# Optimization experiments

Measured on AMD Instinct MI355X. Metric: run time of the kernel, lower is better.

The kernel has to match this reference:

```python
import jax, jax.numpy as jnp
import numpy as np

EMB = 1024
HEADS = 16
HEAD_DIM = EMB // HEADS
EPS = 1e-5


def setup_inputs() -> dict:
    key = jax.random.key(0)
    ks = jax.random.split(key, 10)
    B, T, D = 2, 2048, EMB
    s = 1.0 / np.sqrt(D)
    inp = {
        "x": jax.random.normal(ks[0], (B, T, D), dtype=jnp.float32),
        "wq": jax.random.normal(ks[1], (D, D), dtype=jnp.float32) * s,
        "bq": jnp.zeros((D,), jnp.float32),
        "wk": jax.random.normal(ks[2], (D, D), dtype=jnp.float32) * s,
        "bk": jnp.zeros((D,), jnp.float32),
        "wv": jax.random.normal(ks[3], (D, D), dtype=jnp.float32) * s,
        "bv": jnp.zeros((D,), jnp.float32),
        "wo": jax.random.normal(ks[4], (D, D), dtype=jnp.float32) * s,
        "bo": jnp.zeros((D,), jnp.float32),
        "gamma": jnp.ones((D,), jnp.float32),
        "beta": jnp.zeros((D,), jnp.float32),
    }
    return inp


def _attention(x, wq, bq, wk, bk, wv, bv, wo, bo, gamma, beta):
    B, T, D = x.shape
    H, Hd = HEADS, HEAD_DIM
    q = (x @ wq + bq).reshape(B, T, H, Hd)
    k = (x @ wk + bk).reshape(B, T, H, Hd)
    v = (x @ wv + bv).reshape(B, T, H, Hd)
    # scores: [B, H, T, T]
    scores = jnp.einsum("bthd,bshd->bhts", q, k) / np.sqrt(Hd)
    attn = jax.nn.softmax(scores, axis=-1)  # dropout is identity in eval
    ctx = jnp.einsum("bhts,bshd->bthd", attn, v).reshape(B, T, D)
    out = ctx @ wo + bo
    y = x + out  # residual (dropout identity)
    mu = jnp.mean(y, axis=-1, keepdims=True)
    var = jnp.var(y, axis=-1, keepdims=True)
    return (y - mu) * jax.lax.rsqrt(var + EPS) * gamma + beta


def reference(x, wq, bq, wk, bk, wv, bv, wo, bo, gamma, beta):
    return _attention(x, wq, bq, wk, bk, wv, bv, wo, bo, gamma, beta)
```

## Files before the change

kernel.cpp:

```cpp
#include <hip/hip_runtime.h>

#define BSZ   2
#define TSEQ  2048
#define DMOD  1024
#define NHEAD 16
#define HDIM  64
#define MROW  (BSZ*TSEQ)
#define LNEPS 1e-5f
#define QSCALE 0.18033688011f

typedef __bf16 bf16x8 __attribute__((ext_vector_type(8)));
typedef float  f32x4  __attribute__((ext_vector_type(4)));
typedef unsigned short us8 __attribute__((ext_vector_type(8)));
typedef unsigned short us4 __attribute__((ext_vector_type(4)));

__device__ __forceinline__ unsigned short f2bf(float f) {
    unsigned u = __float_as_uint(f);
    u += 0x7FFF + ((u >> 16) & 1);
    return (unsigned short)(u >> 16);
}
__device__ __forceinline__ float bf2f(unsigned short u) {
    return __uint_as_float((unsigned)u << 16);
}

__device__ __forceinline__ float fexp2(float x) {
#if __has_builtin(__builtin_amdgcn_exp2f)
    return __builtin_amdgcn_exp2f(x);
#else
    return __expf(x * 0.6931471805599453f);
#endif
}

__device__ __forceinline__ void gld_lds16(const void* g, void* l) {
    __builtin_amdgcn_global_load_lds(
        (const __attribute__((address_space(1))) unsigned int*)g,
        (__attribute__((address_space(3))) unsigned int*)l, 16, 0, 0);
}

__global__ __launch_bounds__(256) void prep_k(
    const float* __restrict__ x,
    const float* __restrict__ wq, const float* __restrict__ wk,
    const float* __restrict__ wv, const float* __restrict__ wo,
    unsigned short* __restrict__ Xb,
    unsigned short* __restrict__ WqkvT, unsigned short* __restrict__ WoT)
{
    const int tid = threadIdx.x;
    if (blockIdx.x < 2048) {
        const size_t i = ((size_t)blockIdx.x * 256 + tid) * 8;
        float4 a = *(const float4*)&x[i];
        float4 b = *(const float4*)&x[i + 4];
        union { unsigned short u[8]; uint4 v; } o;
        o.u[0]=f2bf(a.x); o.u[1]=f2bf(a.y); o.u[2]=f2bf(a.z); o.u[3]=f2bf(a.w);
        o.u[4]=f2bf(b.x); o.u[5]=f2bf(b.y); o.u[6]=f2bf(b.z); o.u[7]=f2bf(b.w);
        *(uint4*)&Xb[i] = o.v;
        return;
    }
    __shared__ float T[64][68];
    const int id = blockIdx.x - 2048;
    const int z  = id >> 8;
    const int bx = id & 15;
    const int by = (id >> 4) & 15;
    const float* W = (z == 0) ? wq : (z == 1) ? wk : (z == 2) ? wv : wo;
    unsigned short* Wt = (z < 3) ? (WqkvT + (size_t)z*1024*1024) : WoT;
    const int lr = tid >> 4, lc = (tid & 15) * 4;
    #pragma unroll
    for (int p = 0; p < 4; ++p) {
        const int kk = p*16 + lr;
        float4 v = *(const float4*)&W[(size_t)(by*64 + kk)*1024 + bx*64 + lc];
        T[lc+0][kk] = v.x; T[lc+1][kk] = v.y; T[lc+2][kk] = v.z; T[lc+3][kk] = v.w;
    }
    __syncthreads();
    #pragma unroll
    for (int p = 0; p < 2; ++p) {
        const int nl = p*32 + (tid >> 3);
        const int kb = (tid & 7) * 8;
        float4 a = *(const float4*)&T[nl][kb];
        float4 b = *(const float4*)&T[nl][kb+4];
        union { unsigned short u[8]; uint4 v; } o;
        o.u[0]=f2bf(a.x); o.u[1]=f2bf(a.y); o.u[2]=f2bf(a.z); o.u[3]=f2bf(a.w);
        o.u[4]=f2bf(b.x); o.u[5]=f2bf(b.y); o.u[6]=f2bf(b.z); o.u[7]=f2bf(b.w);
        *(uint4*)&Wt[(size_t)(bx*64 + nl)*1024 + by*64 + kb] = o.v;
    }
}

struct GemmFrags {
    const unsigned short* Ag[4]; const unsigned short* Bg[4];
    unsigned short *la[4], *lb[4];
    const unsigned short *ap[4][2], *bp[4][2];
};

__device__ __forceinline__ void gemm_setup(
    GemmFrags& F, unsigned short* As, unsigned short* Bs,
    const unsigned short* A, const unsigned short* Bt,
    int bm, int bn, int lda)
{
    const int tid  = threadIdx.x;
    const int wv   = tid >> 6;
    const int lane = tid & 63;
    const int quad = lane >> 4;
    const int l16  = lane & 15;
    const int wm   = wv & 1, wn = wv >> 1;
    const int r_l = lane >> 3;
    const int c_l = lane & 7;
    #pragma unroll
    for (int s = 0; s < 4; ++s) {
        const int i = wv*4 + s;
        const int R = i*8 + r_l;
        const int gc = (c_l ^ (R & 7)) * 8;
        F.Ag[s] = A  + (size_t)(bm + R)*lda + gc;
        F.Bg[s] = Bt + (size_t)(bn + R)*lda + gc;
        F.la[s] = As + i*512;
        F.lb[s] = Bs + i*512;
    }
    #pragma unroll
    for (int t = 0; t < 4; ++t)
        #pragma unroll
        for (int kh = 0; kh < 2; ++kh) {
            const int ra = wm*64 + t*16 + l16;
            const int rb = wn*64 + t*16 + l16;
            F.ap[t][kh] = &As[ra*64 + ((kh*4 + quad) ^ (ra & 7))*8];
            F.bp[t][kh] = &Bs[rb*64 + ((kh*4 + quad) ^ (rb & 7))*8];
        }
}

__device__ __forceinline__ void gemm_kloop(
    GemmFrags& F, f32x4 (&acc)[4][4], int k_begin, int k_end)
{
    for (int k0 = k_begin; k0 < k_end; k0 += 64) {
        __syncthreads();
        #pragma unroll
        for (int s = 0; s < 4; ++s) {
            gld_lds16(F.Ag[s] + k0, F.la[s]);
            gld_lds16(F.Bg[s] + k0, F.lb[s]);
        }
        __syncthreads();
        #pragma unroll
        for (int kh = 0; kh < 2; ++kh) {
            bf16x8 af[4], bfr[4];
            #pragma unroll
            for (int t = 0; t < 4; ++t) {
                af[t]  = *(const bf16x8*)F.ap[t][kh];
                bfr[t] = *(const bf16x8*)F.bp[t][kh];
            }
            #pragma unroll
            for (int i = 0; i < 4; ++i)
                #pragma unroll
                for (int j = 0; j < 4; ++j)
                    acc[i][j] = __builtin_amdgcn_mfma_f32_16x16x32_bf16(af[i], bfr[j], acc[i][j], 0, 0, 0);
        }
    }
}

__global__ __launch_bounds__(256) void gemm_qkv_k(
    const unsigned short* __restrict__ A, const unsigned short* __restrict__ Bt,
    const float* __restrict__ b0, const float* __restrict__ b1,
    const float* __restrict__ b2,
    unsigned short* __restrict__ oQ, unsigned short* __restrict__ oK,
    unsigned short* __restrict__ oV)
{
    __shared__ unsigned short As[128*64];
    __shared__ unsigned short Bs[128*64];
    const int tid  = threadIdx.x;
    const int wv   = tid >> 6;
    const int lane = tid & 63;
    const int quad = lane >> 4;
    const int l16  = lane & 15;
    const int wm   = wv & 1, wn = wv >> 1;
    const int bm = blockIdx.y * 128, bn = blockIdx.x * 128;

    GemmFrags F;
    gemm_setup(F, As, Bs, A, Bt, bm, bn, 1024);

    f32x4 acc[4][4];
    #pragma unroll
    for (int i = 0; i < 4; ++i)
        #pragma unroll
        for (int j = 0; j < 4; ++j) acc[i][j] = (f32x4){0.f,0.f,0.f,0.f};

    gemm_kloop(F, acc, 0, 1024);

    const int seg = bn >> 10;
    const float* bias = (seg == 0) ? b0 : (seg == 1) ? b1 : b2;
    const int cb = bn & 1023;
    if (seg < 2) {
        unsigned short* O = (seg == 0) ? oQ : oK;
        const float sc = (seg == 0) ? QSCALE : 1.0f;
        #pragma unroll
        for (int nt = 0; nt < 4; ++nt) {
            const int col = cb + wn*64 + nt*16 + l16;
            const float bs = bias[col];
            #pragma unroll
            for (int mt = 0; mt < 4; ++mt)
                #pragma unroll
                for (int r = 0; r < 4; ++r) {
                    const int grow = bm + wm*64 + mt*16 + quad*4 + r;
                    O[(size_t)grow*1024 + col] = f2bf((acc[mt][nt][r] + bs) * sc);
                }
        }
    } else {
        #pragma unroll
        for (int nt = 0; nt < 4; ++nt) {
            const int ch = cb + wn*64 + nt*16 + l16;
            const float bs = bias[ch];
            #pragma unroll
            for (int mt = 0; mt < 4; ++mt) {
                const int grow0 = bm + wm*64 + mt*16 + quad*4;
                us4 o;
                #pragma unroll
                for (int r = 0; r < 4; ++r) o[r] = f2bf(acc[mt][nt][r] + bs);
                *(us4*)&oV[(size_t)ch*MROW + grow0] = o;
            }
        }
    }
}

__global__ __launch_bounds__(256) void gemm_proj_k(
    const unsigned short* __restrict__ A, const unsigned short* __restrict__ Bt,
    unsigned short* __restrict__ P)
{
    __shared__ unsigned short As[128*64];
    __shared__ unsigned short Bs[128*64];
    const int tid  = threadIdx.x;
    const int wv   = tid >> 6;
    const int lane = tid & 63;
    const int quad = lane >> 4;
    const int l16  = lane & 15;
    const int wm   = wv & 1, wn = wv >> 1;
    const int bm = blockIdx.y * 128, bn = blockIdx.x * 128;
    const int kz = blockIdx.z;

    GemmFrags F;
    gemm_setup(F, As, Bs, A, Bt, bm, bn, 1024);

    f32x4 acc[4][4];
    #pragma unroll
    for (int i = 0; i < 4; ++i)
        #pragma unroll
        for (int j = 0; j < 4; ++j) acc[i][j] = (f32x4){0.f,0.f,0.f,0.f};

    gemm_kloop(F, acc, kz*512, kz*512 + 512);

    unsigned short* O = P + (size_t)kz*MROW*1024;
    #pragma unroll
    for (int nt = 0; nt < 4; ++nt) {
        const int col = bn + wn*64 + nt*16 + l16;
        #pragma unroll
        for (int mt = 0; mt < 4; ++mt)
            #pragma unroll
            for (int r = 0; r < 4; ++r) {
                const int grow = bm + wm*64 + mt*16 + quad*4 + r;
                O[(size_t)grow*1024 + col] = f2bf(acc[mt][nt][r]);
            }
    }
}

__global__ __launch_bounds__(256, 2) void attn_k(
    const unsigned short* __restrict__ Qg,
    const unsigned short* __restrict__ Kg,
    const unsigned short* __restrict__ Vtg,
    unsigned short* __restrict__ CTX)
{
    __shared__ __align__(16) char lds_raw[51200];
    unsigned short* Qs = (unsigned short*)lds_raw;
    unsigned short* Ks = (unsigned short*)(lds_raw + 18432);
    unsigned short* Vs = (unsigned short*)(lds_raw + 34816);
    float* Od = (float*)lds_raw;
    float* Ld = (float*)(lds_raw + 34816);

    const int tid  = threadIdx.x;
    const int wv   = tid >> 6;
    const int lane = tid & 63;
    const int quad = lane >> 4;
    const int l16  = lane & 15;
    const int wq   = wv & 1;
    const int wk   = wv >> 1;
    const int qb   = blockIdx.x * 128;
    const int h    = blockIdx.y;
    const int b    = blockIdx.z;

    {
        const int row = tid & 127, cb = (tid >> 7) * 32;
        const unsigned short* Qrow = Qg + ((size_t)(b*TSEQ + qb + row))*DMOD + h*HDIM + cb;
        #pragma unroll
        for (int j = 0; j < 4; ++j)
            *(us8*)&Qs[row*72 + cb + j*8] = *(const us8*)&Qrow[j*8];
    }
    __syncthreads();
    bf16x8 qf[4][2];
    #pragma unroll
    for (int nt = 0; nt < 4; ++nt)
        #pragma unroll
        for (int kh = 0; kh < 2; ++kh)
            qf[nt][kh] = *(const bf16x8*)&Qs[(wq*64 + nt*16 + l16)*72 + kh*32 + quad*8];

    const int sr = lane >> 3;
    const int sc = lane & 7;
    const bool isK = (wv < 2);
    const int half = wv & 1;
    const unsigned short* gbase;
    unsigned int goff[8];
    unsigned short* ldst;
    if (isK) {
        gbase = Kg + ((size_t)(b*TSEQ + half*1024))*DMOD + h*HDIM;
        #pragma unroll
        for (int s = 0; s < 8; ++s) {
            const int R = s*8 + sr;
            const int gc = sc ^ ((R ^ (R >> 2)) & 7);
            goff[s] = (unsigned)(R*DMOD + gc*8);
        }
        ldst = Ks + half*4096;
    } else {
        gbase = Vtg + ((size_t)(h*HDIM))*MROW + b*TSEQ + half*1024;
        #pragma unroll
        for (int s = 0; s < 8; ++s) {
            const int D = s*8 + sr;
            const int gc = sc ^ (D & 7);
            goff[s] = (unsigned)(D*MROW + gc*8);
        }
        ldst = Vs + half*4096;
    }
    const size_t gstep = isK ? (size_t)64*DMOD : (size_t)64;

    const int rowA_l = (l16 >> 2)*8 + (l16 & 3);
    const int rowB_l = rowA_l + 4;
    const int swA = (rowA_l ^ (rowA_l >> 2)) & 7;
    const int swB = (rowB_l ^ (rowB_l >> 2)) & 7;
    const unsigned short* KsW = Ks + wk*4096;
    const unsigned short* VsW = Vs + wk*4096;

    bf16x8 onef;
    { union { unsigned short u[8]; bf16x8 v; } o1;
      #pragma unroll
      for (int i = 0; i < 8; ++i) o1.u[i] = 0x3F80;
      onef = o1.v; }

    f32x4 oacc[4][4];
    f32x4 lacc[4];
    #pragma unroll
    for (int dt = 0; dt < 4; ++dt)
        #pragma unroll
        for (int nt = 0; nt < 4; ++nt) oacc[dt][nt] = (f32x4){0.f,0.f,0.f,0.f};
    #pragma unroll
    for (int nt = 0; nt < 4; ++nt) lacc[nt] = (f32x4){0.f,0.f,0.f,0.f};

    for (int it = 0; it < 16; ++it) {
        __syncthreads();
        #pragma unroll
        for (int s = 0; s < 8; ++s)
            gld_lds16(gbase + (size_t)it*gstep + goff[s], ldst + s*512);
        __syncthreads();

        #pragma unroll
        for (int gl = 0; gl < 2; ++gl) {
            const int rA = gl*32 + rowA_l;
            const int rB = gl*32 + rowB_l;
            bf16x8 ka0 = *(const bf16x8*)&KsW[rA*64 + ((quad     ^ swA))*8];
            bf16x8 ka1 = *(const bf16x8*)&KsW[rA*64 + (((4+quad) ^ swA))*8];
            bf16x8 kb0 = *(const bf16x8*)&KsW[rB*64 + ((quad     ^ swB))*8];
            bf16x8 kb1 = *(const bf16x8*)&KsW[rB*64 + (((4+quad) ^ swB))*8];
            bf16x8 vf[4];
            #pragma unroll
            for (int dt = 0; dt < 4; ++dt)
                vf[dt] = *(const bf16x8*)&VsW[(dt*16 + l16)*64 + ((gl*4 + quad) ^ (l16 & 7))*8];

            #pragma unroll
            for (int nt = 0; nt < 4; ++nt) {
                f32x4 z = (f32x4){0.f,0.f,0.f,0.f};
                z = __builtin_amdgcn_mfma_f32_16x16x32_bf16(ka0, qf[nt][0], z, 0, 0, 0);
                f32x4 sA = __builtin_amdgcn_mfma_f32_16x16x32_bf16(ka1, qf[nt][1], z, 0, 0, 0);
                z = (f32x4){0.f,0.f,0.f,0.f};
                z = __builtin_amdgcn_mfma_f32_16x16x32_bf16(kb0, qf[nt][0], z, 0, 0, 0);
                f32x4 sB = __builtin_amdgcn_mfma_f32_16x16x32_bf16(kb1, qf[nt][1], z, 0, 0, 0);

                float eA[4], eB[4];
                #pragma unroll
                for (int r = 0; r < 4; ++r) { eA[r] = fexp2(sA[r]); eB[r] = fexp2(sB[r]); }
                union { unsigned d[4]; bf16x8 v; } up;
                up.d[0] = __builtin_amdgcn_perm(__float_as_uint(eA[1]), __float_as_uint(eA[0]), 0x07060302);
                up.d[1] = __builtin_amdgcn_perm(__float_as_uint(eA[3]), __float_as_uint(eA[2]), 0x07060302);
                up.d[2] = __builtin_amdgcn_perm(__float_as_uint(eB[1]), __float_as_uint(eB[0]), 0x07060302);
                up.d[3] = __builtin_amdgcn_perm(__float_as_uint(eB[3]), __float_as_uint(eB[2]), 0x07060302);
                const bf16x8 pf = up.v;

                lacc[nt] = __builtin_amdgcn_mfma_f32_16x16x32_bf16(onef, pf, lacc[nt], 0, 0, 0);
                #pragma unroll
                for (int dt = 0; dt < 4; ++dt)
                    oacc[dt][nt] = __builtin_amdgcn_mfma_f32_16x16x32_bf16(vf[dt], pf, oacc[dt][nt], 0, 0, 0);
            }
        }
    }

    __syncthreads();
    if (wk == 0) {
        float* od = Od + wq*64*68;
        #pragma unroll
        for (int nt = 0; nt < 4; ++nt) {
            #pragma unroll
            for (int dt = 0; dt < 4; ++dt)
                *(f32x4*)&od[(nt*16 + l16)*68 + dt*16 + quad*4] = oacc[dt][nt];
            if (quad == 0) Ld[wq*64 + nt*16 + l16] = lacc[nt][0];
        }
    }
    __syncthreads();
    if (wk == 1) {
        const float* od = Od + wq*64*68;
        #pragma unroll
        for (int nt = 0; nt < 4; ++nt) {
            const float l = Ld[wq*64 + nt*16 + l16] + lacc[nt][0];
            const float inv = 1.f / l;
            const int q = qb + wq*64 + nt*16 + l16;
            unsigned short* crow = CTX + ((size_t)(b*TSEQ + q))*DMOD + h*HDIM;
            #pragma unroll
            for (int dt = 0; dt < 4; ++dt) {
                f32x4 p = *(const f32x4*)&od[(nt*16 + l16)*68 + dt*16 + quad*4];
                us4 o;
                #pragma unroll
                for (int r = 0; r < 4; ++r) o[r] = f2bf((p[r] + oacc[dt][nt][r]) * inv);
                *(us4*)&crow[dt*16 + quad*4] = o;
            }
        }
    }
}

__global__ __launch_bounds__(256) void red_ln_k(
    const float* __restrict__ x, const unsigned short* __restrict__ P,
    const float* __restrict__ bo,
    const float* __restrict__ gamma, const float* __restrict__ beta,
    float* __restrict__ out)
{
    __shared__ float rs[4], rss[4];
    const int row = blockIdx.x;
    const int tid = threadIdx.x;
    const int c = tid * 4;
    const float4 xv = *(const float4*)&x[(size_t)row*DMOD + c];
    const us4 p0 = *(const us4*)&P[(size_t)row*DMOD + c];
    const us4 p1 = *(const us4*)&P[(size_t)(MROW + row)*DMOD + c];
    const float4 bv4 = *(const float4*)&bo[c];
    const float v0 = xv.x + bf2f(p0[0]) + bf2f(p1[0]) + bv4.x;
    const float v1 = xv.y + bf2f(p0[1]) + bf2f(p1[1]) + bv4.y;
    const float v2 = xv.z + bf2f(p0[2]) + bf2f(p1[2]) + bv4.z;
    const float v3 = xv.w + bf2f(p0[3]) + bf2f(p1[3]) + bv4.w;
    float s  = v0 + v1 + v2 + v3;
    float ss = v0*v0 + v1*v1 + v2*v2 + v3*v3;
    #pragma unroll
    for (int o = 32; o > 0; o >>= 1) {
        s  += __shfl_down(s,  o, 64);
        ss += __shfl_down(ss, o, 64);
    }
    if ((tid & 63) == 0) { rs[tid >> 6] = s; rss[tid >> 6] = ss; }
    __syncthreads();
    s  = rs[0] + rs[1] + rs[2] + rs[3];
    ss = rss[0] + rss[1] + rss[2] + rss[3];
    const float mean = s * (1.f/DMOD);
    const float var  = ss * (1.f/DMOD) - mean*mean;
    const float rstd = rsqrtf(var + LNEPS);
    const float4 gv = *(const float4*)&gamma[c];
    const float4 bv = *(const float4*)&beta[c];
    float4 o;
    o.x = (v0 - mean)*rstd*gv.x + bv.x;
    o.y = (v1 - mean)*rstd*gv.y + bv.y;
    o.z = (v2 - mean)*rstd*gv.z + bv.z;
    o.w = (v3 - mean)*rstd*gv.w + bv.w;
    *(float4*)&out[(size_t)row*DMOD + c] = o;
}

extern "C" void kernel_launch(void* const* d_in, const int* in_sizes, int n_in,
                              void* d_out, int out_size, void* d_ws, size_t ws_size,
                              hipStream_t stream) {
    const float* x     = (const float*)d_in[0];
    const float* wq    = (const float*)d_in[1];
    const float* bq    = (const float*)d_in[2];
    const float* wk    = (const float*)d_in[3];
    const float* bk    = (const float*)d_in[4];
    const float* wvp   = (const float*)d_in[5];
    const float* bvp   = (const float*)d_in[6];
    const float* wo    = (const float*)d_in[7];
    const float* bo    = (const float*)d_in[8];
    const float* gamma = (const float*)d_in[9];
    const float* beta  = (const float*)d_in[10];
    float* out = (float*)d_out;

    unsigned short* Xb    = (unsigned short*)d_ws;
    unsigned short* WqkvT = Xb    + (size_t)MROW*DMOD;
    unsigned short* WoT   = WqkvT + (size_t)3072*1024;
    unsigned short* Qb    = WoT   + (size_t)1024*1024;
    unsigned short* Kb    = Qb    + (size_t)MROW*DMOD;
    unsigned short* VtG   = Kb    + (size_t)MROW*DMOD;
    unsigned short* CTXb  = VtG   + (size_t)DMOD*MROW;
    unsigned short* Pp    = Qb;

    prep_k<<<3072, 256, 0, stream>>>(x, wq, wk, wvp, wo, Xb, WqkvT, WoT);

    gemm_qkv_k<<<dim3(3072/128, MROW/128), 256, 0, stream>>>(
        Xb, WqkvT, bq, bk, bvp, Qb, Kb, VtG);

    attn_k<<<dim3(TSEQ/128, NHEAD, BSZ), 256, 0, stream>>>(Qb, Kb, VtG, CTXb);

    gemm_proj_k<<<dim3(DMOD/128, MROW/128, 2), 256, 0, stream>>>(CTXb, WoT, Pp);

    red_ln_k<<<MROW, 256, 0, stream>>>(x, Pp, bo, gamma, beta, out);
}
```

Before: 196.5 us.

## Rewrite QKV and projection GEMMs as 256x256 double-buffered 8-wave pipelined kernels

Replaces the 128x128 single-buffered GEMM core with a 256x256 tile computed by 512 threads (8 waves). It uses 128 KB of dynamic LDS for double-buffered A/B K-slabs, interleaving async global-to-LDS loads with MFMA phases under barrier scheduling and s_setprio. Block indices are remapped with a grouped swizzle to improve L2 reuse. The intent is to hide global load latency and raise MFMA utilisation. The risks are fewer blocks (192 and 128) on a 256-CU part, lower occupancy from the large LDS footprint, and fragile manual waitcnt accounting.

```diff
diff --git a/kernel.cpp b/kernel.cpp
--- a/kernel.cpp
+++ b/kernel.cpp
@@ -83,173 +83,256 @@
     }
 }
 
-struct GemmFrags {
-    const unsigned short* Ag[4]; const unsigned short* Bg[4];
-    unsigned short *la[4], *lb[4];
-    const unsigned short *ap[4][2], *bp[4][2];
+
+#define PH_SYNC() do { __builtin_amdgcn_s_barrier(); \
+    asm volatile("s_waitcnt lgkmcnt(0)" ::: "memory"); \
+    __builtin_amdgcn_sched_barrier(0); } while (0)
+
+struct Core8 {
+    const unsigned short *sA, *sB;
+    unsigned short *A0w, *A1w, *B0w, *B1w;
+    const unsigned short *fA0, *fA1, *fB0, *fB1;
+    int swz0, swz1;
 };
 
-__device__ __forceinline__ void gemm_setup(
-    GemmFrags& F, unsigned short* As, unsigned short* Bs,
-    const unsigned short* A, const unsigned short* Bt,
-    int bm, int bn, int lda)
-{
-    const int tid  = threadIdx.x;
-    const int wv   = tid >> 6;
-    const int lane = tid & 63;
-    const int quad = lane >> 4;
-    const int l16  = lane & 15;
-    const int wm   = wv & 1, wn = wv >> 1;
-    const int r_l = lane >> 3;
-    const int c_l = lane & 7;
-    #pragma unroll
-    for (int s = 0; s < 4; ++s) {
-        const int i = wv*4 + s;
-        const int R = i*8 + r_l;
-        const int gc = (c_l ^ (R & 7)) * 8;
-        F.Ag[s] = A  + (size_t)(bm + R)*lda + gc;
-        F.Bg[s] = Bt + (size_t)(bn + R)*lda + gc;
-        F.la[s] = As + i*512;
-        F.lb[s] = Bs + i*512;
-    }
-    #pragma unroll
-    for (int t = 0; t < 4; ++t)
-        #pragma unroll
-        for (int kh = 0; kh < 2; ++kh) {
-            const int ra = wm*64 + t*16 + l16;
-            const int rb = wn*64 + t*16 + l16;
-            F.ap[t][kh] = &As[ra*64 + ((kh*4 + quad) ^ (ra & 7))*8];
-            F.bp[t][kh] = &Bs[rb*64 + ((kh*4 + quad) ^ (rb & 7))*8];
-        }
-}
-
-__device__ __forceinline__ void gemm_kloop(
-    GemmFrags& F, f32x4 (&acc)[4][4], int k_begin, int k_end)
-{
-    for (int k0 = k_begin; k0 < k_end; k0 += 64) {
-        __syncthreads();
-        #pragma unroll
-        for (int s = 0; s < 4; ++s) {
-            gld_lds16(F.Ag[s] + k0, F.la[s]);
-            gld_lds16(F.Bg[s] + k0, F.lb[s]);
-        }
-        __syncthreads();
-        #pragma unroll
-        for (int kh = 0; kh < 2; ++kh) {
-            bf16x8 af[4], bfr[4];
-            #pragma unroll
-            for (int t = 0; t < 4; ++t) {
-                af[t]  = *(const bf16x8*)F.ap[t][kh];
-                bfr[t] = *(const bf16x8*)F.bp[t][kh];
-            }
-            #pragma unroll
-            for (int i = 0; i < 4; ++i)
-                #pragma unroll
-                for (int j = 0; j < 4; ++j)
-                    acc[i][j] = __builtin_amdgcn_mfma_f32_16x16x32_bf16(af[i], bfr[j], acc[i][j], 0, 0, 0);
-        }
-    }
-}
-
-__global__ __launch_bounds__(256) void gemm_qkv_k(
+__device__ __forceinline__ void stage2(const unsigned short* s, unsigned short* d) {
+    gld_lds16(s, d);
+    gld_lds16(s + 64*1024, d + 4096);
+}
+
+__device__ __forceinline__ void core_setup(Core8& C, unsigned short* LDS,
+    const unsigned short* A, const unsigned short* Bt, int bm, int bn, int kbase)
+{
+    const int tid = threadIdx.x;
+    const int w = tid >> 6, lane = tid & 63;
+    const int quad = lane >> 4, l16 = lane & 15;
+    const int wm = w >> 2, wn = w & 3;
+    const int r_l = lane >> 3, c_l = lane & 7;
+    C.sA = A  + (size_t)(bm + w*8 + r_l)*1024 + (c_l ^ r_l)*8 + kbase;
+    C.sB = Bt + (size_t)(bn + w*8 + r_l)*1024 + (c_l ^ r_l)*8 + kbase;
+    unsigned short* A0 = LDS;
+    unsigned short* A1 = LDS + 16384;
+    unsigned short* B0 = LDS + 32768;
+    unsigned short* B1 = LDS + 49152;
+    C.A0w = A0 + w*512; C.A1w = A1 + w*512;
+    C.B0w = B0 + w*512; C.B1w = B1 + w*512;
+    C.fA0 = A0 + (wm*128 + l16)*64; C.fA1 = A1 + (wm*128 + l16)*64;
+    C.fB0 = B0 + (wn*64 + l16)*64;  C.fB1 = B1 + (wn*64 + l16)*64;
+    C.swz0 = ( quad      ^ (l16 & 7)) * 8;
+    C.swz1 = ((4 + quad) ^ (l16 & 7)) * 8;
+}
+
+__device__ __forceinline__ void ld_b(const Core8& C, bf16x8 (&bfr)[4][2],
+                                     const unsigned short* fB) {
+    #pragma unroll
+    for (int n = 0; n < 4; ++n) {
+        bfr[n][0] = *(const bf16x8*)(fB + n*1024 + C.swz0);
+        bfr[n][1] = *(const bf16x8*)(fB + n*1024 + C.swz1);
+    }
+}
+
+template<int Q>
+__device__ __forceinline__ void ld_a(const Core8& C, bf16x8 (&af)[2][2],
+                                     const unsigned short* fA) {
+    #pragma unroll
+    for (int dm = 0; dm < 2; ++dm) {
+        af[dm][0] = *(const bf16x8*)(fA + (Q*2+dm)*1024 + C.swz0);
+        af[dm][1] = *(const bf16x8*)(fA + (Q*2+dm)*1024 + C.swz1);
+    }
+}
+
+template<int Q>
+__device__ __forceinline__ void mma_q(f32x4 (&acc)[8][4], bf16x8 (&af)[2][2],
+                                      bf16x8 (&bfr)[4][2]) {
+    __builtin_amdgcn_s_setprio(1);
+    #pragma unroll
+    for (int dm = 0; dm < 2; ++dm)
+        #pragma unroll
+        for (int n = 0; n < 4; ++n) {
+            f32x4 t = acc[Q*2+dm][n];
+            t = __builtin_amdgcn_mfma_f32_16x16x32_bf16(af[dm][0], bfr[n][0], t, 0, 0, 0);
+            t = __builtin_amdgcn_mfma_f32_16x16x32_bf16(af[dm][1], bfr[n][1], t, 0, 0, 0);
+            acc[Q*2+dm][n] = t;
+        }
+    __builtin_amdgcn_s_setprio(0);
+}
+
+template<int NIT>
+__device__ __forceinline__ void core_kloop(const Core8& C, f32x4 (&acc)[8][4])
+{
+    stage2(C.sA,                 C.A0w);
+    stage2(C.sA + 128*1024,      C.A0w + 8192);
+    stage2(C.sB,                 C.B0w);
+    stage2(C.sB + 128*1024,      C.B0w + 8192);
+    stage2(C.sB + 64,            C.B1w);
+    stage2(C.sB + 128*1024 + 64, C.B1w + 8192);
+    asm volatile("s_waitcnt vmcnt(4)" ::: "memory");
+    __builtin_amdgcn_s_barrier();
+
+    bf16x8 bfr[4][2];
+    bf16x8 af[2][2];
+
+    #pragma unroll 1
+    for (int it = 0; it < NIT - 1; ++it) {
+        const int kk = it * 128;
+        ld_b(C, bfr, C.fB0);
+        ld_a<0>(C, af, C.fA0);
+        stage2(C.sA + kk + 64,            C.A1w);
+        stage2(C.sA + 128*1024 + kk + 64, C.A1w + 8192);
+        PH_SYNC();  mma_q<0>(acc, af, bfr);
+        __builtin_amdgcn_s_barrier();
+        ld_a<1>(C, af, C.fA0);
+        stage2(C.sB + kk + 128, C.B0w);
+        PH_SYNC();  mma_q<1>(acc, af, bfr);
+        __builtin_amdgcn_s_barrier();
+        ld_a<2>(C, af, C.fA0);
+        stage2(C.sB + 128*1024 + kk + 128, C.B0w + 8192);
+        PH_SYNC();  mma_q<2>(acc, af, bfr);
+        __builtin_amdgcn_s_barrier();
+        ld_a<3>(C, af, C.fA0);
+        PH_SYNC();  mma_q<3>(acc, af, bfr);
+        asm volatile("s_waitcnt vmcnt(4)" ::: "memory");
+        __builtin_amdgcn_s_barrier();
+        ld_b(C, bfr, C.fB1);
+        ld_a<0>(C, af, C.fA1);
+        stage2(C.sA + kk + 128,            C.A0w);
+        stage2(C.sA + 128*1024 + kk + 128, C.A0w + 8192);
+        PH_SYNC();  mma_q<0>(acc, af, bfr);
+        __builtin_amdgcn_s_barrier();
+        ld_a<1>(C, af, C.fA1);
+        stage2(C.sB + kk + 192, C.B1w);
+        PH_SYNC();  mma_q<1>(acc, af, bfr);
+        __builtin_amdgcn_s_barrier();
+        ld_a<2>(C, af, C.fA1);
+        stage2(C.sB + 128*1024 + kk + 192, C.B1w + 8192);
+        PH_SYNC();  mma_q<2>(acc, af, bfr);
+        __builtin_amdgcn_s_barrier();
+        ld_a<3>(C, af, C.fA1);
+        PH_SYNC();  mma_q<3>(acc, af, bfr);
+        asm volatile("s_waitcnt vmcnt(4)" ::: "memory");
+        __builtin_amdgcn_s_barrier();
+    }
+
+    {
+        const int kk = (NIT - 1) * 128;
+        ld_b(C, bfr, C.fB0);
+        ld_a<0>(C, af, C.fA0);
+        stage2(C.sA + kk + 64,            C.A1w);
+        stage2(C.sA + 128*1024 + kk + 64, C.A1w + 8192);
+        PH_SYNC();  mma_q<0>(acc, af, bfr);
+        __builtin_amdgcn_s_barrier();
+        ld_a<1>(C, af, C.fA0); PH_SYNC(); mma_q<1>(acc, af, bfr); __builtin_amdgcn_s_barrier();
+        ld_a<2>(C, af, C.fA0); PH_SYNC(); mma_q<2>(acc, af, bfr); __builtin_amdgcn_s_barrier();
+        ld_a<3>(C, af, C.fA0); PH_SYNC(); mma_q<3>(acc, af, bfr);
+        asm volatile("s_waitcnt vmcnt(0)" ::: "memory");
+        __builtin_amdgcn_s_barrier();
+        ld_b(C, bfr, C.fB1);
+        ld_a<0>(C, af, C.fA1); PH_SYNC(); mma_q<0>(acc, af, bfr); __builtin_amdgcn_s_barrier();
+        ld_a<1>(C, af, C.fA1); PH_SYNC(); mma_q<1>(acc, af, bfr); __builtin_amdgcn_s_barrier();
+        ld_a<2>(C, af, C.fA1); PH_SYNC(); mma_q<2>(acc, af, bfr); __builtin_amdgcn_s_barrier();
+        ld_a<3>(C, af, C.fA1); PH_SYNC(); mma_q<3>(acc, af, bfr);
+    }
+}
+
+__global__ __launch_bounds__(512, 2) void gemm_qkv_k(
     const unsigned short* __restrict__ A, const unsigned short* __restrict__ Bt,
     const float* __restrict__ b0, const float* __restrict__ b1,
     const float* __restrict__ b2,
     unsigned short* __restrict__ oQ, unsigned short* __restrict__ oK,
     unsigned short* __restrict__ oV)
 {
-    __shared__ unsigned short As[128*64];
-    __shared__ unsigned short Bs[128*64];
-    const int tid  = threadIdx.x;
-    const int wv   = tid >> 6;
-    const int lane = tid & 63;
-    const int quad = lane >> 4;
-    const int l16  = lane & 15;
-    const int wm   = wv & 1, wn = wv >> 1;
-    const int bm = blockIdx.y * 128, bn = blockIdx.x * 128;
-
-    GemmFrags F;
-    gemm_setup(F, As, Bs, A, Bt, bm, bn, 1024);
-
-    f32x4 acc[4][4];
-    #pragma unroll
-    for (int i = 0; i < 4; ++i)
+    extern __shared__ unsigned short LDS[];
+    const int ob = blockIdx.x;
+    const int wg = (ob & 7) * 24 + (ob >> 3);
+    const int by = wg / 12, bx = wg - by*12;
+    const int bm = by * 256, bn = bx * 256;
+
+    Core8 C;
+    core_setup(C, LDS, A, Bt, bm, bn, 0);
+
+    f32x4 acc[8][4];
+    #pragma unroll
+    for (int i = 0; i < 8; ++i)
         #pragma unroll
         for (int j = 0; j < 4; ++j) acc[i][j] = (f32x4){0.f,0.f,0.f,0.f};
 
-    gemm_kloop(F, acc, 0, 1024);
-
+    core_kloop<8>(C, acc);
+
+    const int tid = threadIdx.x;
+    const int w = tid >> 6, lane = tid & 63;
+    const int quad = lane >> 4, l16 = lane & 15;
+    const int wm = w >> 2, wn = w & 3;
     const int seg = bn >> 10;
-    const float* bias = (seg == 0) ? b0 : (seg == 1) ? b1 : b2;
-    const int cb = bn & 1023;
+    const int cb  = bn & 1023;
     if (seg < 2) {
         unsigned short* O = (seg == 0) ? oQ : oK;
         const float sc = (seg == 0) ? QSCALE : 1.0f;
-        #pragma unroll
-        for (int nt = 0; nt < 4; ++nt) {
-            const int col = cb + wn*64 + nt*16 + l16;
+        const float* bias = (seg == 0) ? b0 : b1;
+        #pragma unroll
+        for (int n = 0; n < 4; ++n) {
+            const int col = cb + wn*64 + n*16 + l16;
             const float bs = bias[col];
             #pragma unroll
-            for (int mt = 0; mt < 4; ++mt)
+            for (int m = 0; m < 8; ++m)
                 #pragma unroll
                 for (int r = 0; r < 4; ++r) {
-                    const int grow = bm + wm*64 + mt*16 + quad*4 + r;
-                    O[(size_t)grow*1024 + col] = f2bf((acc[mt][nt][r] + bs) * sc);
+                    const int grow = bm + wm*128 + m*16 + quad*4 + r;
+                    O[(size_t)grow*1024 + col] = f2bf((acc[m][n][r] + bs) * sc);
                 }
         }
     } else {
         #pragma unroll
-        for (int nt = 0; nt < 4; ++nt) {
-            const int ch = cb + wn*64 + nt*16 + l16;
-            const float bs = bias[ch];
-            #pragma unroll
-            for (int mt = 0; mt < 4; ++mt) {
-                const int grow0 = bm + wm*64 + mt*16 + quad*4;
+        for (int n = 0; n < 4; ++n) {
+            const int ch = cb + wn*64 + n*16 + l16;
+            const float bs = b2[ch];
+            #pragma unroll
+            for (int m = 0; m < 8; ++m) {
+                const int grow0 = bm + wm*128 + m*16 + quad*4;
                 us4 o;
                 #pragma unroll
-                for (int r = 0; r < 4; ++r) o[r] = f2bf(acc[mt][nt][r] + bs);
+                for (int r = 0; r < 4; ++r) o[r] = f2bf(acc[m][n][r] + bs);
                 *(us4*)&oV[(size_t)ch*MROW + grow0] = o;
             }
         }
     }
 }
 
-__global__ __launch_bounds__(256) void gemm_proj_k(
+__global__ __launch_bounds__(512, 2) void gemm_proj_k(
     const unsigned short* __restrict__ A, const unsigned short* __restrict__ Bt,
     unsigned short* __restrict__ P)
 {
-    __shared__ unsigned short As[128*64];
-    __shared__ unsigned short Bs[128*64];
-    const int tid  = threadIdx.x;
-    const int wv   = tid >> 6;
-    const int lane = tid & 63;
-    const int quad = lane >> 4;
-    const int l16  = lane & 15;
-    const int wm   = wv & 1, wn = wv >> 1;
-    const int bm = blockIdx.y * 128, bn = blockIdx.x * 128;
-    const int kz = blockIdx.z;
-
-    GemmFrags F;
-    gemm_setup(F, As, Bs, A, Bt, bm, bn, 1024);
-
-    f32x4 acc[4][4];
-    #pragma unroll
-    for (int i = 0; i < 4; ++i)
+    extern __shared__ unsigned short LDS[];
+    const int ob = blockIdx.x;
+    const int wg = (ob & 7) * 8 + (ob >> 3);
+    const int by = wg >> 2, bx = wg & 3;
+    const int kz = blockIdx.y;
+    const int bm = by * 256, bn = bx * 256;
+
+    Core8 C;
+    core_setup(C, LDS, A, Bt, bm, bn, kz * 512);
+
+    f32x4 acc[8][4];
+    #pragma unroll
+    for (int i = 0; i < 8; ++i)
         #pragma unroll
         for (int j = 0; j < 4; ++j) acc[i][j] = (f32x4){0.f,0.f,0.f,0.f};
 
-    gemm_kloop(F, acc, kz*512, kz*512 + 512);
-
+    core_kloop<4>(C, acc);
+
+    const int tid = threadIdx.x;
+    const int w = tid >> 6, lane = tid & 63;
+    const int quad = lane >> 4, l16 = lane & 15;
+    const int wm = w >> 2, wn = w & 3;
     unsigned short* O = P + (size_t)kz*MROW*1024;
     #pragma unroll
-    for (int nt = 0; nt < 4; ++nt) {
-        const int col = bn + wn*64 + nt*16 + l16;
-        #pragma unroll
-        for (int mt = 0; mt < 4; ++mt)
+    for (int n = 0; n < 4; ++n) {
+        const int col = bn + wn*64 + n*16 + l16;
+        #pragma unroll
+        for (int m = 0; m < 8; ++m)
             #pragma unroll
             for (int r = 0; r < 4; ++r) {
-                const int grow = bm + wm*64 + mt*16 + quad*4 + r;
-                O[(size_t)grow*1024 + col] = f2bf(acc[mt][nt][r]);
+                const int grow = bm + wm*128 + m*16 + quad*4 + r;
+                O[(size_t)grow*1024 + col] = f2bf(acc[m][n][r]);
             }
     }
 }
@@ -491,12 +574,12 @@
 
     prep_k<<<3072, 256, 0, stream>>>(x, wq, wk, wvp, wo, Xb, WqkvT, WoT);
 
-    gemm_qkv_k<<<dim3(3072/128, MROW/128), 256, 0, stream>>>(
+    gemm_qkv_k<<<dim3(192), 512, 131072, stream>>>(
         Xb, WqkvT, bq, bk, bvp, Qb, Kb, VtG);
 
     attn_k<<<dim3(TSEQ/128, NHEAD, BSZ), 256, 0, stream>>>(Qb, Kb, VtG, CTXb);
 
-    gemm_proj_k<<<dim3(DMOD/128, MROW/128, 2), 256, 0, stream>>>(CTXb, WoT, Pp);
+    gemm_proj_k<<<dim3(64, 2), 512, 131072, stream>>>(CTXb, WoT, Pp);
 
     red_ln_k<<<MROW, 256, 0, stream>>>(x, Pp, bo, gamma, beta, out);
 }
```

After: 194.2 us. About the same (-1.2%).
